# Optimization experiments

Measured on AMD Instinct MI355X. Metric: run time of the kernel, lower is better.

The kernel has to match this reference:

```python
import jax, jax.numpy as jnp
import numpy as np

LN_EPS = 1e-5

def _layernorm(x, g, b):
    mu = jnp.mean(x, axis=-1, keepdims=True)
    var = jnp.var(x, axis=-1, keepdims=True)
    return (x - mu) * jax.lax.rsqrt(var + LN_EPS) * g + b

def setup_inputs() -> dict:
    key = jax.random.key(0)
    ks = jax.random.split(key, 8)
    B, L, d_atom, d_hid = 8, 128, 256, 32
    return {
        "z":    jax.random.normal(ks[0], (B, L, d_atom), dtype=jnp.float32),
        "W_in": jax.random.normal(ks[1], (d_atom, 2 * d_hid), dtype=jnp.float32) * 0.02,
        "b_in": jnp.zeros((2 * d_hid,), dtype=jnp.float32),
        "ln_g": jnp.ones((2 * d_hid,), dtype=jnp.float32),
        "ln_b": jnp.zeros((2 * d_hid,), dtype=jnp.float32),
        "W1":   jax.random.normal(ks[2], (d_hid * d_hid, 21), dtype=jnp.float32) * 0.02,
        "b1":   jnp.zeros((21,), dtype=jnp.float32),
        "W2":   jax.random.normal(ks[3], (d_hid * d_hid, 30), dtype=jnp.float32) * 0.02,
        "b2":   jnp.zeros((30,), dtype=jnp.float32),
    }

def reference(z, W_in, b_in, ln_g, ln_b, W1, b1, W2, b2):
    # linear_in: Linear -> exact GELU -> LayerNorm
    ab = _layernorm(jax.nn.gelu(z @ W_in + b_in, approximate=False), ln_g, ln_b)
    h = ab.shape[-1] // 2
    a, b = ab[..., :h], ab[..., h:]              # (B, L, h) each
    # Fused bilinear form: outer(a_l, b_m) flattened to h*h, then Linear.
    # Equivalent to materializing (B, L, L, h*h) and matmul, reassociated.
    W1r = W1.reshape(h, h, -1)                   # (h, h, 21)
    W2r = W2.reshape(h, h, -1)                   # (h, h, 30)
    x1 = jnp.einsum('blc,bmd,cdk->blmk', a, b, W1r) + b1  # (B, L, L, 21)
    x2 = jnp.einsum('blc,bmd,cdk->blmk', a, b, W2r) + b2  # (B, L, L, 30)
    return (x1, x2)
```

## Files before the change

### kernel.cpp

```cpp
#include <hip/hip_runtime.h>
#include <hip/hip_bf16.h>
#include <math.h>

#define NB 8
#define NL 128
#define D_ATOM 256
#define DH 32
#define DAB 64
#define K1 21
#define K2 30
#define KT 51
#define ROWS (NB*NL)
#define LN_EPS 1e-5f

#define OUT1_ROW (NL*K1)
#define OUT2_ROW (NL*K2)
#define STAGE_N  (OUT1_ROW + OUT2_ROW)

typedef __attribute__((ext_vector_type(8))) short bf16x8;
typedef __attribute__((ext_vector_type(4))) float f32x4;

__device__ __forceinline__ unsigned short f2bf(float x) {
    __hip_bfloat16 h = __float2bfloat16(x);
    return *reinterpret_cast<unsigned short*>(&h);
}

__global__ __launch_bounds__(256) void ln_kernel(
    const float* __restrict__ z, const float* __restrict__ W_in,
    const float* __restrict__ b_in, const float* __restrict__ ln_g,
    const float* __restrict__ ln_b, float* __restrict__ a_out,
    float* __restrict__ b_out)
{
    __shared__ float Wl[D_ATOM * DAB];
    __shared__ float zl[4][D_ATOM];
    const int t = threadIdx.x;
    const int w = t >> 6, j = t & 63;
    const int row0 = blockIdx.x * 4;

    #pragma unroll
    for (int s = 0; s < 16; ++s) {
        int i4 = t + s * 256;
        ((float4*)Wl)[i4] = ((const float4*)W_in)[i4];
    }
    ((float4*)zl)[t] = ((const float4*)(z + (size_t)row0 * D_ATOM))[t];
    __syncthreads();

    float acc = b_in[j];
    #pragma unroll 8
    for (int i = 0; i < D_ATOM; ++i)
        acc = fmaf(zl[w][i], Wl[i * DAB + j], acc);

    float g = 0.5f * acc * (1.0f + erff(acc * 0.70710678118654752f));

    float s = g, sq = g * g;
    #pragma unroll
    for (int msk = 1; msk < 64; msk <<= 1) {
        s  += __shfl_xor(s,  msk, 64);
        sq += __shfl_xor(sq, msk, 64);
    }
    float mu  = s  * (1.0f / 64.0f);
    float var = sq * (1.0f / 64.0f) - mu * mu;
    float y = (g - mu) * rsqrtf(var + LN_EPS) * ln_g[j] + ln_b[j];

    const int row = row0 + w;
    if (j < DH) a_out[row * DH + j]        = y;
    else        b_out[row * DH + (j - DH)] = y;
}

__global__ __launch_bounds__(256) void pair_mfma_kernel(
    const float* __restrict__ a_g, const float* __restrict__ b_g,
    const float* __restrict__ W1, const float* __restrict__ b1v,
    const float* __restrict__ W2, const float* __restrict__ b2v,
    float* __restrict__ out)
{
    const int row0  = blockIdx.x * 2;
    const int batch = row0 >> 7;
    const int t     = threadIdx.x;

    __shared__ unsigned short bbf[8 * 64 * 8];
    __shared__ unsigned short Tf[2 * 4 * 64 * 8];
    __shared__ float a_lds[2][DH];
    __shared__ __align__(16) float stg[2][STAGE_N];

    if (t < 2 * DH) a_lds[t >> 5][t & 31] = a_g[row0 * DH + t];

    #pragma unroll
    for (int s = 0; s < 8; ++s)
        ((unsigned int*)Tf)[t + s * 256] = 0u;

    #pragma unroll
    for (int s = 0; s < 2; ++s) {
        int e = t + s * 256;
        int mt = e >> 6, l = e & 63;
        int m = mt * 16 + (l & 15), d0 = (l >> 4) * 8;
        const float4* p = (const float4*)(b_g + ((size_t)batch * NL + m) * DH + d0);
        float4 v0 = p[0], v1 = p[1];
        uint4 wv;
        wv.x = (unsigned)f2bf(v0.x) | ((unsigned)f2bf(v0.y) << 16);
        wv.y = (unsigned)f2bf(v0.z) | ((unsigned)f2bf(v0.w) << 16);
        wv.z = (unsigned)f2bf(v1.x) | ((unsigned)f2bf(v1.y) << 16);
        wv.w = (unsigned)f2bf(v1.z) | ((unsigned)f2bf(v1.w) << 16);
        ((uint4*)bbf)[e] = wv;
    }
    __syncthreads();

    float tacc0[7], tacc1[7];
    const float* wptr[7];
    int wstr[7], fidx[7];
    bool val[7];
    #pragma unroll
    for (int s = 0; s < 7; ++s) {
        int o = t + s * 256;
        val[s] = (o < 1632);
        int oo = val[s] ? o : 0;
        int d, k;
        if (oo < 672) {
            wptr[s] = W1 + oo; wstr[s] = 672;
            d = oo / 21; k = oo % 21;
        } else {
            int o2 = oo - 672;
            wptr[s] = W2 + o2; wstr[s] = 960;
            d = o2 / 30; k = 21 + o2 % 30;
        }
        int kt = k >> 4, lane = (k & 15) | ((d >> 3) << 4), reg = d & 7;
        fidx[s] = (kt * 64 + lane) * 8 + reg;
        tacc0[s] = 0.f; tacc1[s] = 0.f;
    }
    #pragma unroll 4
    for (int c = 0; c < DH; ++c) {
        float ac0 = a_lds[0][c], ac1 = a_lds[1][c];
        #pragma unroll
        for (int s = 0; s < 7; ++s) {
            float w = wptr[s][c * wstr[s]];
            tacc0[s] = fmaf(ac0, w, tacc0[s]);
            tacc1[s] = fmaf(ac1, w, tacc1[s]);
        }
    }
    #pragma unroll
    for (int s = 0; s < 7; ++s) {
        if (val[s]) {
            Tf[fidx[s]]        = f2bf(tacc0[s]);
            Tf[2048 + fidx[s]] = f2bf(tacc1[s]);
        }
    }
    __syncthreads();

    const int w  = t >> 6, l = t & 63;
    const int r  = w >> 1;
    const int mh = w & 1;

    bf16x8 af[4], bfr[4];
    #pragma unroll
    for (int i = 0; i < 4; ++i)
        af[i] = ((const bf16x8*)bbf)[(mh * 4 + i) * 64 + l];
    #pragma unroll
    for (int kt = 0; kt < 4; ++kt)
        bfr[kt] = ((const bf16x8*)Tf)[(r * 4 + kt) * 64 + l];

    float bias[4];
    #pragma unroll
    for (int kt = 0; kt < 4; ++kt) {
        int k = kt * 16 + (l & 15);
        bias[kt] = (k < K1) ? b1v[k] : (k < KT ? b2v[k - K1] : 0.f);
    }

    #pragma unroll
    for (int i = 0; i < 4; ++i) {
        const int mbase = (mh * 4 + i) * 16 + (l >> 4) * 4;
        #pragma unroll
        for (int kt = 0; kt < 4; ++kt) {
            f32x4 acc = __builtin_amdgcn_mfma_f32_16x16x32_bf16(
                af[i], bfr[kt], (f32x4){0.f, 0.f, 0.f, 0.f}, 0, 0, 0);
            const int k = kt * 16 + (l & 15);
            if (k < K1) {
                #pragma unroll
                for (int q = 0; q < 4; ++q)
                    stg[r][(mbase + q) * K1 + k] = acc[q] + bias[kt];
            } else if (k < KT) {
                #pragma unroll
                for (int q = 0; q < 4; ++q)
                    stg[r][OUT1_ROW + (mbase + q) * K2 + (k - K1)] = acc[q] + bias[kt];
            }
        }
    }
    __syncthreads();

    #pragma unroll
    for (int rr = 0; rr < 2; ++rr) {
        const int row = row0 + rr;
        float* o1 = out + (size_t)row * OUT1_ROW;
        float* o2 = out + (size_t)ROWS * OUT1_ROW + (size_t)row * OUT2_ROW;
        const float4* s1 = (const float4*)stg[rr];
        const float4* s2 = (const float4*)(stg[rr] + OUT1_ROW);
        for (int i4 = t; i4 < OUT1_ROW / 4; i4 += 256)
            ((float4*)o1)[i4] = s1[i4];
        for (int i4 = t; i4 < OUT2_ROW / 4; i4 += 256)
            ((float4*)o2)[i4] = s2[i4];
    }
}

extern "C" void kernel_launch(void* const* d_in, const int* in_sizes, int n_in,
                              void* d_out, int out_size, void* d_ws, size_t ws_size,
                              hipStream_t stream) {
    const float* z    = (const float*)d_in[0];
    const float* W_in = (const float*)d_in[1];
    const float* b_in = (const float*)d_in[2];
    const float* ln_g = (const float*)d_in[3];
    const float* ln_b = (const float*)d_in[4];
    const float* W1   = (const float*)d_in[5];
    const float* b1   = (const float*)d_in[6];
    const float* W2   = (const float*)d_in[7];
    const float* b2   = (const float*)d_in[8];
    float* out = (float*)d_out;

    float* a_ws = (float*)d_ws;
    float* b_ws = a_ws + ROWS * DH;

    ln_kernel<<<ROWS / 4, 256, 0, stream>>>(z, W_in, b_in, ln_g, ln_b, a_ws, b_ws);
    pair_mfma_kernel<<<ROWS / 2, 256, 0, stream>>>(a_ws, b_ws, W1, b1, W2, b2, out);
}
```

Measured before the change: 23.94 us.

## Compute per-row T=a·W via separate MFMA GEMM kernel with prepacked bf16 operands

The per-row contraction of a with W1/W2 (previously scalar FMAs repeated in every pair block, reading strided fp32 weights) moves into its own kernel that runs one bf16 MFMA GEMM over all rows. The first kernel now also writes a and b in the MFMA fragment layout as bf16, and extra blocks repack W1/W2 into bf16 fragment layout. The pair kernel just loads the precomputed fragments from global memory. This drops the redundant per-block weight reads and LDS setup, at the cost of a third launch and a workspace round trip for T.

```diff
diff --git a/kernel.cpp b/kernel.cpp
--- a/kernel.cpp
+++ b/kernel.cpp
@@ -17,6 +17,9 @@
 #define OUT2_ROW (NL*K2)
 #define STAGE_N  (OUT1_ROW + OUT2_ROW)
 
+#define NTILES 104
+#define TROW_HW 2048
+
 typedef __attribute__((ext_vector_type(8))) short bf16x8;
 typedef __attribute__((ext_vector_type(4))) float f32x4;
 
@@ -25,15 +28,34 @@
     return *reinterpret_cast<unsigned short*>(&h);
 }
 
-__global__ __launch_bounds__(256) void ln_kernel(
+__global__ __launch_bounds__(256) void ln_wprep_kernel(
     const float* __restrict__ z, const float* __restrict__ W_in,
     const float* __restrict__ b_in, const float* __restrict__ ln_g,
-    const float* __restrict__ ln_b, float* __restrict__ a_out,
-    float* __restrict__ b_out)
+    const float* __restrict__ ln_b, const float* __restrict__ W1,
+    const float* __restrict__ W2, unsigned short* __restrict__ af,
+    unsigned short* __restrict__ bbf, unsigned short* __restrict__ Wf)
 {
+    const int t = threadIdx.x;
+
+    if (blockIdx.x >= 256) {
+        const int base = ((int)blockIdx.x - 256) * 4096;
+        #pragma unroll
+        for (int e = 0; e < 16; ++e) {
+            int widx = base + e * 256 + t;
+            int nt = widx >> 9, lane = (widx >> 3) & 63, reg = widx & 7;
+            int dk = nt * 16 + (lane & 15);
+            int c  = ((lane >> 4) << 3) + reg;
+            int d  = dk / 52, k = dk - d * 52;
+            float v = 0.f;
+            if (k < K1)      v = W1[(c * DH + d) * K1 + k];
+            else if (k < KT) v = W2[(c * DH + d) * K2 + (k - K1)];
+            Wf[widx] = f2bf(v);
+        }
+        return;
+    }
+
     __shared__ float Wl[D_ATOM * DAB];
     __shared__ float zl[4][D_ATOM];
-    const int t = threadIdx.x;
     const int w = t >> 6, j = t & 63;
     const int row0 = blockIdx.x * 4;
 
@@ -63,99 +85,65 @@
     float y = (g - mu) * rsqrtf(var + LN_EPS) * ln_g[j] + ln_b[j];
 
     const int row = row0 + w;
-    if (j < DH) a_out[row * DH + j]        = y;
-    else        b_out[row * DH + (j - DH)] = y;
-}
-
-__global__ __launch_bounds__(256) void pair_mfma_kernel(
-    const float* __restrict__ a_g, const float* __restrict__ b_g,
-    const float* __restrict__ W1, const float* __restrict__ b1v,
-    const float* __restrict__ W2, const float* __restrict__ b2v,
+    unsigned short hv = f2bf(y);
+    if (j < DH) {
+        const int c = j;
+        af[((row >> 4) << 9) + ((((row & 15) | ((c >> 3) << 4)) << 3) | (c & 7))] = hv;
+    } else {
+        const int d = j - DH, m = row & 127, batch = row >> 7;
+        bbf[batch * 4096 + ((m >> 4) << 9) +
+            ((((m & 15) | ((d >> 3) << 4)) << 3) | (d & 7))] = hv;
+    }
+}
+
+__global__ __launch_bounds__(256) void t_gemm_kernel(
+    const unsigned short* __restrict__ af, const unsigned short* __restrict__ Wf,
+    unsigned short* __restrict__ T_ws)
+{
+    const int mt = blockIdx.x;
+    const int w  = threadIdx.x >> 6, l = threadIdx.x & 63;
+
+    const bf16x8 a = ((const bf16x8*)af)[mt * 64 + l];
+    const int rowb = mt * 16 + ((l >> 4) << 2);
+
+    for (int i = 0; i < 26; ++i) {
+        const int nt = w * 26 + i;
+        const bf16x8 b = ((const bf16x8*)Wf)[nt * 64 + l];
+        f32x4 c = __builtin_amdgcn_mfma_f32_16x16x32_bf16(
+            a, b, (f32x4){0.f, 0.f, 0.f, 0.f}, 0, 0, 0);
+        const int dk = nt * 16 + (l & 15);
+        const int d = dk / 52, k = dk - d * 52;
+        if (k < KT) {
+            const int off = ((k >> 4) << 9) +
+                            ((((k & 15) | ((d >> 3) << 4)) << 3) | (d & 7));
+            #pragma unroll
+            for (int q = 0; q < 4; ++q)
+                T_ws[(size_t)(rowb + q) * TROW_HW + off] = f2bf(c[q]);
+        }
+    }
+}
+
+__global__ __launch_bounds__(256) void pair_kernel(
+    const unsigned short* __restrict__ bbf, const unsigned short* __restrict__ T_ws,
+    const float* __restrict__ b1v, const float* __restrict__ b2v,
     float* __restrict__ out)
 {
     const int row0  = blockIdx.x * 2;
     const int batch = row0 >> 7;
     const int t     = threadIdx.x;
-
-    __shared__ unsigned short bbf[8 * 64 * 8];
-    __shared__ unsigned short Tf[2 * 4 * 64 * 8];
-    __shared__ float a_lds[2][DH];
+    const int w = t >> 6, l = t & 63;
+    const int r = w >> 1;
+    const int mh = w & 1;
+
     __shared__ __align__(16) float stg[2][STAGE_N];
 
-    if (t < 2 * DH) a_lds[t >> 5][t & 31] = a_g[row0 * DH + t];
-
-    #pragma unroll
-    for (int s = 0; s < 8; ++s)
-        ((unsigned int*)Tf)[t + s * 256] = 0u;
-
-    #pragma unroll
-    for (int s = 0; s < 2; ++s) {
-        int e = t + s * 256;
-        int mt = e >> 6, l = e & 63;
-        int m = mt * 16 + (l & 15), d0 = (l >> 4) * 8;
-        const float4* p = (const float4*)(b_g + ((size_t)batch * NL + m) * DH + d0);
-        float4 v0 = p[0], v1 = p[1];
-        uint4 wv;
-        wv.x = (unsigned)f2bf(v0.x) | ((unsigned)f2bf(v0.y) << 16);
-        wv.y = (unsigned)f2bf(v0.z) | ((unsigned)f2bf(v0.w) << 16);
-        wv.z = (unsigned)f2bf(v1.x) | ((unsigned)f2bf(v1.y) << 16);
-        wv.w = (unsigned)f2bf(v1.z) | ((unsigned)f2bf(v1.w) << 16);
-        ((uint4*)bbf)[e] = wv;
-    }
-    __syncthreads();
-
-    float tacc0[7], tacc1[7];
-    const float* wptr[7];
-    int wstr[7], fidx[7];
-    bool val[7];
-    #pragma unroll
-    for (int s = 0; s < 7; ++s) {
-        int o = t + s * 256;
-        val[s] = (o < 1632);
-        int oo = val[s] ? o : 0;
-        int d, k;
-        if (oo < 672) {
-            wptr[s] = W1 + oo; wstr[s] = 672;
-            d = oo / 21; k = oo % 21;
-        } else {
-            int o2 = oo - 672;
-            wptr[s] = W2 + o2; wstr[s] = 960;
-            d = o2 / 30; k = 21 + o2 % 30;
-        }
-        int kt = k >> 4, lane = (k & 15) | ((d >> 3) << 4), reg = d & 7;
-        fidx[s] = (kt * 64 + lane) * 8 + reg;
-        tacc0[s] = 0.f; tacc1[s] = 0.f;
-    }
-    #pragma unroll 4
-    for (int c = 0; c < DH; ++c) {
-        float ac0 = a_lds[0][c], ac1 = a_lds[1][c];
-        #pragma unroll
-        for (int s = 0; s < 7; ++s) {
-            float w = wptr[s][c * wstr[s]];
-            tacc0[s] = fmaf(ac0, w, tacc0[s]);
-            tacc1[s] = fmaf(ac1, w, tacc1[s]);
-        }
-    }
-    #pragma unroll
-    for (int s = 0; s < 7; ++s) {
-        if (val[s]) {
-            Tf[fidx[s]]        = f2bf(tacc0[s]);
-            Tf[2048 + fidx[s]] = f2bf(tacc1[s]);
-        }
-    }
-    __syncthreads();
-
-    const int w  = t >> 6, l = t & 63;
-    const int r  = w >> 1;
-    const int mh = w & 1;
-
-    bf16x8 af[4], bfr[4];
+    bf16x8 afr[4], bfr[4];
     #pragma unroll
     for (int i = 0; i < 4; ++i)
-        af[i] = ((const bf16x8*)bbf)[(mh * 4 + i) * 64 + l];
+        afr[i] = ((const bf16x8*)bbf)[batch * 512 + (mh * 4 + i) * 64 + l];
     #pragma unroll
     for (int kt = 0; kt < 4; ++kt)
-        bfr[kt] = ((const bf16x8*)Tf)[(r * 4 + kt) * 64 + l];
+        bfr[kt] = ((const bf16x8*)T_ws)[(size_t)(row0 + r) * 256 + kt * 64 + l];
 
     float bias[4];
     #pragma unroll
@@ -170,7 +158,7 @@
         #pragma unroll
         for (int kt = 0; kt < 4; ++kt) {
             f32x4 acc = __builtin_amdgcn_mfma_f32_16x16x32_bf16(
-                af[i], bfr[kt], (f32x4){0.f, 0.f, 0.f, 0.f}, 0, 0, 0);
+                afr[i], bfr[kt], (f32x4){0.f, 0.f, 0.f, 0.f}, 0, 0, 0);
             const int k = kt * 16 + (l & 15);
             if (k < K1) {
                 #pragma unroll
@@ -213,9 +201,13 @@
     const float* b2   = (const float*)d_in[8];
     float* out = (float*)d_out;
 
-    float* a_ws = (float*)d_ws;
-    float* b_ws = a_ws + ROWS * DH;
-
-    ln_kernel<<<ROWS / 4, 256, 0, stream>>>(z, W_in, b_in, ln_g, ln_b, a_ws, b_ws);
-    pair_mfma_kernel<<<ROWS / 2, 256, 0, stream>>>(a_ws, b_ws, W1, b1, W2, b2, out);
-}
+    unsigned short* af   = (unsigned short*)d_ws;
+    unsigned short* bbf  = af + 32768;
+    unsigned short* Wf   = bbf + 32768;
+    unsigned short* T_ws = Wf + 53248;
+
+    ln_wprep_kernel<<<269, 256, 0, stream>>>(z, W_in, b_in, ln_g, ln_b,
+                                             W1, W2, af, bbf, Wf);
+    t_gemm_kernel<<<64, 256, 0, stream>>>(af, Wf, T_ws);
+    pair_kernel<<<ROWS / 2, 256, 0, stream>>>(bbf, T_ws, b1, b2, out);
+}
```

Result: slower. 32.14 us (+34.2%).
